# Optimization experiments

Measured on AMD Instinct MI355X. Metric: run time of the kernel, lower is better.

The kernel has to match this reference:

```python
import jax, jax.numpy as jnp
import numpy as np

QUERY_DIM = 1024
KEY_DIM = 768
NUM_HEADS = 16
HEAD_DIM = QUERY_DIM // NUM_HEADS
SCALE = HEAD_DIM ** -0.5


def setup_inputs() -> dict:
    key = jax.random.key(0)
    ks = jax.random.split(key, 11)
    B, Nq, Nk = 4, 4096, 1024
    s_q = QUERY_DIM ** -0.5
    s_k = KEY_DIM ** -0.5
    return {
        "query": jax.random.normal(ks[0], (B, Nq, QUERY_DIM), jnp.float32),
        "key": jax.random.normal(ks[1], (B, Nk, KEY_DIM), jnp.float32),
        "value": jax.random.normal(ks[2], (B, Nk, KEY_DIM), jnp.float32),
        "Wq": jax.random.normal(ks[3], (QUERY_DIM, QUERY_DIM), jnp.float32) * s_q,
        "bq": jnp.zeros((QUERY_DIM,), jnp.float32),
        "Wk": jax.random.normal(ks[4], (KEY_DIM, QUERY_DIM), jnp.float32) * s_k,
        "bk": jnp.zeros((QUERY_DIM,), jnp.float32),
        "Wv": jax.random.normal(ks[5], (KEY_DIM, QUERY_DIM), jnp.float32) * s_k,
        "bv": jnp.zeros((QUERY_DIM,), jnp.float32),
        "Wo": jax.random.normal(ks[6], (QUERY_DIM, QUERY_DIM), jnp.float32) * s_q,
        "bo": jnp.zeros((QUERY_DIM,), jnp.float32),
    }


def reference(query, key, value, Wq, bq, Wk, bk, Wv, bv, Wo, bo):
    B, Nq, _ = query.shape
    Nk = key.shape[1]
    # projections to (B, H, N, d)
    q = (query @ Wq + bq).reshape(B, Nq, NUM_HEADS, HEAD_DIM).transpose(0, 2, 1, 3)
    k = (key @ Wk + bk).reshape(B, Nk, NUM_HEADS, HEAD_DIM).transpose(0, 2, 1, 3)
    v = (value @ Wv + bv).reshape(B, Nk, NUM_HEADS, HEAD_DIM).transpose(0, 2, 1, 3)
    attn = jnp.einsum("bhqd,bhkd->bhqk", q, k) * SCALE
    attn = jax.nn.softmax(attn, axis=-1)
    out = jnp.einsum("bhqk,bhkd->bhqd", attn, v)
    out = out.transpose(0, 2, 1, 3).reshape(B, Nq, QUERY_DIM)
    return out @ Wo + bo
```

## Files before the change

### kernel.cpp

```cpp
#include <hip/hip_runtime.h>
#include <hip/hip_bf16.h>
#include <stdint.h>


typedef unsigned short u16;
typedef __attribute__((ext_vector_type(8))) short short8;
typedef __attribute__((ext_vector_type(4))) float f32x4;

#define B_SZ 4
#define NQ   4096
#define NK   1024
#define QDIM 1024
#define KDIM 768
#define NH   16
#define HD   64
#define QSCALE (0.125f * 1.44269504f)

__device__ __forceinline__ u16 f2bf(float f) {
  union { float f; uint32_t u; } v; v.f = f;
  uint32_t u = v.u;
  return (u16)((u + 0x7FFFu + ((u >> 16) & 1u)) >> 16);
}

__device__ __forceinline__ uint32_t pk2(float a, float b) {
  union { __hip_bfloat162 h; uint32_t u; } cv;
  cv.h = __float22bfloat162_rn(float2{a, b});
  return cv.u;
}

__device__ __forceinline__ float fexp2(float x) {
  return __builtin_amdgcn_exp2f(x);
}

__device__ __forceinline__ void async16(u16* lds, const u16* g) {
  __builtin_amdgcn_global_load_lds(
      (__attribute__((address_space(1))) void*)(g),
      (__attribute__((address_space(3))) void*)(lds), 16, 0, 0);
}

__global__ __launch_bounds__(256) void f32_to_bf16_k(const float* __restrict__ in,
                                                     u16* __restrict__ out, int n4) {
  int i = blockIdx.x * 256 + threadIdx.x;
  if (i < n4) {
    f32x4 v = ((const f32x4*)in)[i];
    uint2 o = {pk2(v.x, v.y), pk2(v.z, v.w)};
    ((uint2*)out)[i] = o;
  }
}

__global__ __launch_bounds__(256) void f32_to_bf16_2k(const float* __restrict__ a,
                                                      const float* __restrict__ b,
                                                      u16* __restrict__ oa,
                                                      u16* __restrict__ ob, int n4) {
  int i = blockIdx.x * 256 + threadIdx.x;
  const float* in = blockIdx.y ? b : a;
  u16* out = blockIdx.y ? ob : oa;
  if (i < n4) {
    f32x4 v = ((const f32x4*)in)[i];
    uint2 o = {pk2(v.x, v.y), pk2(v.z, v.w)};
    ((uint2*)out)[i] = o;
  }
}

__global__ __launch_bounds__(256) void transpose_bf16_k(const float* __restrict__ W,
                                                        u16* __restrict__ Wt,
                                                        int K, int N) {
  __shared__ float t[32][33];
  int tx = threadIdx.x & 31, ty = threadIdx.x >> 5;
  int nb = blockIdx.x * 32, kb = blockIdx.y * 32;
#pragma unroll
  for (int i = 0; i < 4; ++i)
    t[ty + i * 8][tx] = W[(size_t)(kb + ty + i * 8) * N + nb + tx];
  __syncthreads();
#pragma unroll
  for (int i = 0; i < 4; ++i)
    Wt[(size_t)(nb + ty + i * 8) * K + kb + tx] = f2bf(t[tx][ty + i * 8]);
}

__global__ __launch_bounds__(512, 2) void gemm_bt256(const u16* __restrict__ A,
                                                     const u16* __restrict__ Bt,
                                                     const float* __restrict__ bias,
                                                     float* __restrict__ Cf,
                                                     u16* __restrict__ Cb,
                                                     int M, int N, int K,
                                                     int out_bf16, float scale) {
  __shared__ __align__(16) u16 Al[3][128 * 64];
  __shared__ __align__(16) u16 Bl[3][256 * 64];
  const int tid = threadIdx.x;
  const int w = tid >> 6, lane = tid & 63;
  const int g = lane >> 4, l15 = lane & 15;
  const int sw = l15 & 7;
  const int mbase = blockIdx.x * 128, nbase = blockIdx.y * 256;
  const int wm = (w & 1) * 64, wn = (w >> 1) * 64;
  const int NT = K >> 6;

  const int ca0 = 0 * 512 + tid, ca1 = 1 * 512 + tid;
  const int ra0 = ca0 >> 3, rc0 = ((ca0 & 7) ^ (ra0 & 7)) * 8;
  const int ra1 = ca1 >> 3, rc1 = ((ca1 & 7) ^ (ra1 & 7)) * 8;
  const u16* pa0 = A + (size_t)(mbase + ra0) * K + rc0;
  const u16* pa1 = A + (size_t)(mbase + ra1) * K + rc1;
  const u16* pb[4];
#pragma unroll
  for (int i = 0; i < 4; ++i) {
    int c = i * 512 + tid;
    int row = c >> 3, col = ((c & 7) ^ (row & 7)) * 8;
    pb[i] = Bt + (size_t)(nbase + row) * K + col;
  }
  const int lA0 = (0 * 512 + w * 64) * 8, lA1 = (1 * 512 + w * 64) * 8;
  int lB[4];
#pragma unroll
  for (int i = 0; i < 4; ++i) lB[i] = (i * 512 + w * 64) * 8;

  f32x4 zero4 = {0.f, 0.f, 0.f, 0.f};
  f32x4 acc[4][4];
#pragma unroll
  for (int i = 0; i < 4; ++i)
#pragma unroll
    for (int j = 0; j < 4; ++j) acc[i][j] = zero4;

  async16(&Al[0][lA0], pa0); async16(&Al[0][lA1], pa1);
#pragma unroll
  for (int i = 0; i < 4; ++i) async16(&Bl[0][lB[i]], pb[i]);
  pa0 += 64; pa1 += 64;
#pragma unroll
  for (int i = 0; i < 4; ++i) pb[i] += 64;
  async16(&Al[1][lA0], pa0); async16(&Al[1][lA1], pa1);
#pragma unroll
  for (int i = 0; i < 4; ++i) async16(&Bl[1][lB[i]], pb[i]);
  pa0 += 64; pa1 += 64;
#pragma unroll
  for (int i = 0; i < 4; ++i) pb[i] += 64;
  asm volatile("s_waitcnt vmcnt(6)" ::: "memory");
  __builtin_amdgcn_sched_barrier(0);
  __builtin_amdgcn_s_barrier();

  int cb = 0, sb = 2;
  for (int kt = 0; kt < NT; ++kt) {
    const u16* Ap = &Al[cb][0];
    const u16* Bp = &Bl[cb][0];
    const bool st = (kt + 2 < NT);

    short8 af[4][2], bfa[2][2];
#pragma unroll
    for (int mt = 0; mt < 4; ++mt) {
      af[mt][0] = *(const short8*)&Ap[(wm + mt * 16 + l15) * 64 + (g ^ sw) * 8];
      af[mt][1] = *(const short8*)&Ap[(wm + mt * 16 + l15) * 64 + ((4 + g) ^ sw) * 8];
    }
#pragma unroll
    for (int nt = 0; nt < 2; ++nt) {
      bfa[nt][0] = *(const short8*)&Bp[(wn + nt * 16 + l15) * 64 + (g ^ sw) * 8];
      bfa[nt][1] = *(const short8*)&Bp[(wn + nt * 16 + l15) * 64 + ((4 + g) ^ sw) * 8];
    }
    if (st) {
      async16(&Al[sb][lA0], pa0);
      async16(&Al[sb][lA1], pa1);
      async16(&Bl[sb][lB[0]], pb[0]);
      async16(&Bl[sb][lB[1]], pb[1]);
    }
    __builtin_amdgcn_s_barrier();
    asm volatile("s_waitcnt lgkmcnt(0)" ::: "memory");
    __builtin_amdgcn_sched_barrier(0);
    __builtin_amdgcn_s_setprio(1);
#pragma unroll
    for (int ks = 0; ks < 2; ++ks)
#pragma unroll
      for (int mt = 0; mt < 4; ++mt)
#pragma unroll
        for (int nt = 0; nt < 2; ++nt)
          acc[mt][nt] = __builtin_amdgcn_mfma_f32_16x16x32_bf16(af[mt][ks], bfa[nt][ks],
                                                                acc[mt][nt], 0, 0, 0);
    __builtin_amdgcn_s_setprio(0);
    __builtin_amdgcn_s_barrier();

    short8 bfb[2][2];
#pragma unroll
    for (int nt = 0; nt < 2; ++nt) {
      bfb[nt][0] = *(const short8*)&Bp[(wn + (nt + 2) * 16 + l15) * 64 + (g ^ sw) * 8];
      bfb[nt][1] = *(const short8*)&Bp[(wn + (nt + 2) * 16 + l15) * 64 + ((4 + g) ^ sw) * 8];
    }
    if (st) {
      async16(&Bl[sb][lB[2]], pb[2]);
      async16(&Bl[sb][lB[3]], pb[3]);
      pa0 += 64; pa1 += 64;
#pragma unroll
      for (int i = 0; i < 4; ++i) pb[i] += 64;
    }
    __builtin_amdgcn_s_barrier();
    asm volatile("s_waitcnt lgkmcnt(0)" ::: "memory");
    __builtin_amdgcn_sched_barrier(0);
    __builtin_amdgcn_s_setprio(1);
#pragma unroll
    for (int ks = 0; ks < 2; ++ks)
#pragma unroll
      for (int mt = 0; mt < 4; ++mt)
#pragma unroll
        for (int nt = 0; nt < 2; ++nt)
          acc[mt][nt + 2] = __builtin_amdgcn_mfma_f32_16x16x32_bf16(af[mt][ks], bfb[nt][ks],
                                                                    acc[mt][nt + 2], 0, 0, 0);
    __builtin_amdgcn_s_setprio(0);

    if (kt < NT - 2) {
      asm volatile("s_waitcnt vmcnt(6)" ::: "memory");
    } else if (kt == NT - 2) {
      asm volatile("s_waitcnt vmcnt(0)" ::: "memory");
    }
    __builtin_amdgcn_sched_barrier(0);
    __builtin_amdgcn_s_barrier();
    cb = (cb == 2) ? 0 : cb + 1;
    sb = (sb == 2) ? 0 : sb + 1;
  }

#pragma unroll
  for (int nt = 0; nt < 4; ++nt) {
    int col = nbase + wn + nt * 16 + l15;
    float bv = bias[col];
#pragma unroll
    for (int mt = 0; mt < 4; ++mt)
#pragma unroll
      for (int r = 0; r < 4; ++r) {
        int row = mbase + wm + mt * 16 + g * 4 + r;
        float v = (acc[mt][nt][r] + bv) * scale;
        if (out_bf16) Cb[(size_t)row * N + col] = f2bf(v);
        else          Cf[(size_t)row * N + col] = v;
      }
  }
}

__global__ __launch_bounds__(256) void gemm_kv(const u16* __restrict__ kA,
                                               const u16* __restrict__ vA,
                                               const u16* __restrict__ Wk,
                                               const u16* __restrict__ Wv,
                                               const float* __restrict__ bk,
                                               const float* __restrict__ bv,
                                               u16* __restrict__ Kp,
                                               u16* __restrict__ VT,
                                               int M, int N, int K) {
  __shared__ __align__(16) u16 Al[128 * 64];
  __shared__ __align__(16) u16 Bl[128 * 64];
  const int ct = blockIdx.z;
  const u16* A  = ct ? vA : kA;
  const u16* Bt = ct ? Wv : Wk;
  const float* bias = ct ? bv : bk;
  const int tid = threadIdx.x;
  const int w = tid >> 6, lane = tid & 63;
  const int g = lane >> 4, l15 = lane & 15;
  const int sw = l15 & 7;
  const int mbase = blockIdx.x * 128, nbase = blockIdx.y * 128;
  const int wm = (w & 1) * 64, wn = (w >> 1) * 64;

  f32x4 zero4 = {0.f, 0.f, 0.f, 0.f};
  f32x4 acc[4][4];
#pragma unroll
  for (int i = 0; i < 4; ++i)
#pragma unroll
    for (int j = 0; j < 4; ++j) acc[i][j] = zero4;

  for (int kb = 0; kb < K; kb += 64) {
#pragma unroll
    for (int i = 0; i < 4; ++i) {
      int cbase = w * 256 + i * 64;
      int c = cbase + lane;
      int row = c >> 3;
      int kc8 = ((c & 7) ^ (row & 7)) * 8;
      async16(&Al[cbase * 8], A + (size_t)(mbase + row) * K + kb + kc8);
      async16(&Bl[cbase * 8], Bt + (size_t)(nbase + row) * K + kb + kc8);
    }
    __syncthreads();
#pragma unroll
    for (int ks = 0; ks < 2; ++ks) {
      short8 af[4], bf[4];
#pragma unroll
      for (int mt = 0; mt < 4; ++mt)
        af[mt] = *(const short8*)&Al[(wm + mt * 16 + l15) * 64 + ((ks * 4 + g) ^ sw) * 8];
#pragma unroll
      for (int nt = 0; nt < 4; ++nt)
        bf[nt] = *(const short8*)&Bl[(wn + nt * 16 + l15) * 64 + ((ks * 4 + g) ^ sw) * 8];
      if (ct) {
#pragma unroll
        for (int nt = 0; nt < 4; ++nt)
#pragma unroll
          for (int mt = 0; mt < 4; ++mt)
            acc[nt][mt] = __builtin_amdgcn_mfma_f32_16x16x32_bf16(bf[nt], af[mt],
                                                                  acc[nt][mt], 0, 0, 0);
      } else {
#pragma unroll
        for (int mt = 0; mt < 4; ++mt)
#pragma unroll
          for (int nt = 0; nt < 4; ++nt)
            acc[mt][nt] = __builtin_amdgcn_mfma_f32_16x16x32_bf16(af[mt], bf[nt],
                                                                  acc[mt][nt], 0, 0, 0);
      }
    }
    __syncthreads();
  }

  if (ct) {
#pragma unroll
    for (int mt = 0; mt < 4; ++mt) {
      int m = mbase + wm + mt * 16 + l15;
#pragma unroll
      for (int nt = 0; nt < 4; ++nt)
#pragma unroll
        for (int r = 0; r < 4; ++r) {
          int n = nbase + wn + nt * 16 + g * 4 + r;
          VT[(size_t)n * M + m] = f2bf(acc[nt][mt][r] + bias[n]);
        }
    }
  } else {
#pragma unroll
    for (int nt = 0; nt < 4; ++nt) {
      int col = nbase + wn + nt * 16 + l15;
      float bvv = bias[col];
#pragma unroll
      for (int mt = 0; mt < 4; ++mt)
#pragma unroll
        for (int r = 0; r < 4; ++r) {
          int row = mbase + wm + mt * 16 + g * 4 + r;
          Kp[(size_t)row * N + col] = f2bf(acc[mt][nt][r] + bvv);
        }
    }
  }
}

__global__ __launch_bounds__(256, 2) void attn_kernel(const u16* __restrict__ Qp,
                                                      const u16* __restrict__ Kp,
                                                      const u16* __restrict__ VT,
                                                      u16* __restrict__ AO) {
  __shared__ __align__(16) u16 K_lds[2][64 * 64];
  __shared__ __align__(16) u16 V_lds[3][64 * 64];
  __shared__ __align__(16) u16 P_lds[4][32 * 64];

  const int tid = threadIdx.x;
  const int w = tid >> 6, lane = tid & 63;
  const int g = lane >> 4, l15 = lane & 15;
  const int sw = l15 & 7;
  const int bh = blockIdx.y, b = bh >> 4, h = bh & 15;
  const int qrow0 = blockIdx.x * 128 + w * 32;
  const int MT = B_SZ * NK;

  const int cbase0 = (w * 2 + 0) * 64;
  const int cbase1 = (w * 2 + 1) * 64;
  const int c0 = cbase0 + lane, c1 = cbase1 + lane;
  const int row0 = c0 >> 3, kc80 = ((c0 & 7) ^ (row0 & 7)) * 8;
  const int row1 = c1 >> 3, kc81 = ((c1 & 7) ^ (row1 & 7)) * 8;

  const u16* kp0 = Kp + (size_t)(b * NK + row0) * QDIM + h * HD + kc80;
  const u16* kp1 = Kp + (size_t)(b * NK + row1) * QDIM + h * HD + kc81;
  const u16* vp0 = VT + (size_t)(h * HD + row0) * MT + b * NK + kc80;
  const u16* vp1 = VT + (size_t)(h * HD + row1) * MT + b * NK + kc81;

  const int rb = l15 * 64;
  const int cs0 = (g ^ sw) * 8;
  const int cs1 = ((4 + g) ^ sw) * 8;
  const int pwb = rb + (((g >> 1) ^ (sw & 1)) * 8) + (g & 1) * 4;
  const int pms = sw & 6;

  short8 ones8;
#pragma unroll
  for (int j = 0; j < 8; ++j) ones8[j] = (short)0x3F80;

  short8 qf[2][2];
#pragma unroll
  for (int qt = 0; qt < 2; ++qt)
#pragma unroll
    for (int ks = 0; ks < 2; ++ks) {
      size_t row = (size_t)(b * NQ + qrow0 + qt * 16 + l15);
      qf[qt][ks] = *(const short8*)(Qp + row * QDIM + h * HD + ks * 32 + g * 8);
    }

  f32x4 zero4 = {0.f, 0.f, 0.f, 0.f};
  f32x4 o4[4][2];
  f32x4 lacc[2];
#pragma unroll
  for (int dt = 0; dt < 4; ++dt)
#pragma unroll
    for (int qt = 0; qt < 2; ++qt) o4[dt][qt] = zero4;
  lacc[0] = zero4; lacc[1] = zero4;

  u16* Pl = &P_lds[w][0];

  async16(&K_lds[0][cbase0 * 8], kp0);
  async16(&K_lds[0][cbase1 * 8], kp1);
  async16(&V_lds[0][cbase0 * 8], vp0);
  async16(&V_lds[0][cbase1 * 8], vp1);
  kp0 += 64 * QDIM; kp1 += 64 * QDIM; vp0 += 64; vp1 += 64;
  __syncthreads();

  async16(&K_lds[1][cbase0 * 8], kp0);
  async16(&K_lds[1][cbase1 * 8], kp1);
  async16(&V_lds[1][cbase0 * 8], vp0);
  async16(&V_lds[1][cbase1 * 8], vp1);
  kp0 += 64 * QDIM; kp1 += 64 * QDIM; vp0 += 64; vp1 += 64;

  {
    const u16* Kl = &K_lds[0][0];
    f32x4 sc[4][2];
    short8 kf0[4], kf1[4];
#pragma unroll
    for (int mt = 0; mt < 4; ++mt) {
      kf0[mt] = *(const short8*)&Kl[mt * 1024 + rb + cs0];
      kf1[mt] = *(const short8*)&Kl[mt * 1024 + rb + cs1];
    }
    __builtin_amdgcn_s_setprio(1);
#pragma unroll
    for (int mt = 0; mt < 4; ++mt)
#pragma unroll
      for (int qt = 0; qt < 2; ++qt)
        sc[mt][qt] = __builtin_amdgcn_mfma_f32_16x16x32_bf16(kf0[mt], qf[qt][0],
                                                             zero4, 0, 0, 0);
#pragma unroll
    for (int mt = 0; mt < 4; ++mt)
#pragma unroll
      for (int qt = 0; qt < 2; ++qt)
        sc[mt][qt] = __builtin_amdgcn_mfma_f32_16x16x32_bf16(kf1[mt], qf[qt][1],
                                                             sc[mt][qt], 0, 0, 0);
    __builtin_amdgcn_s_setprio(0);
#pragma unroll
    for (int qt = 0; qt < 2; ++qt)
#pragma unroll
      for (int mt = 0; mt < 4; ++mt) {
        float p0 = fexp2(sc[mt][qt][0]);
        float p1 = fexp2(sc[mt][qt][1]);
        float p2 = fexp2(sc[mt][qt][2]);
        float p3 = fexp2(sc[mt][qt][3]);
        uint2 pk = {pk2(p0, p1), pk2(p2, p3)};
        *(uint2*)&Pl[qt * 1024 + pwb + ((mt * 2) ^ pms) * 8] = pk;
      }
  }
  __syncthreads();

  for (int kc = 1; kc < NK / 64; ++kc) {
    const int pv = (kc - 1) % 3;
    if (kc + 1 < NK / 64) {
      const int nk = (kc + 1) & 1, nv = (kc + 1) % 3;
      async16(&K_lds[nk][cbase0 * 8], kp0);
      async16(&K_lds[nk][cbase1 * 8], kp1);
      async16(&V_lds[nv][cbase0 * 8], vp0);
      async16(&V_lds[nv][cbase1 * 8], vp1);
      kp0 += 64 * QDIM; kp1 += 64 * QDIM; vp0 += 64; vp1 += 64;
    }
    const u16* Kl = &K_lds[kc & 1][0];
    const u16* Vl = &V_lds[pv][0];

    short8 pb[2][2], vf[2][4], kf[2][4];
#pragma unroll
    for (int qt = 0; qt < 2; ++qt) {
      pb[0][qt] = *(const short8*)&Pl[qt * 1024 + rb + cs0];
      pb[1][qt] = *(const short8*)&Pl[qt * 1024 + rb + cs1];
    }
#pragma unroll
    for (int dt = 0; dt < 4; ++dt) {
      vf[0][dt] = *(const short8*)&Vl[dt * 1024 + rb + cs0];
      vf[1][dt] = *(const short8*)&Vl[dt * 1024 + rb + cs1];
    }
#pragma unroll
    for (int mt = 0; mt < 4; ++mt) {
      kf[0][mt] = *(const short8*)&Kl[mt * 1024 + rb + cs0];
      kf[1][mt] = *(const short8*)&Kl[mt * 1024 + rb + cs1];
    }

    f32x4 sc[4][2];
    __builtin_amdgcn_s_setprio(1);
#pragma unroll
    for (int mt = 0; mt < 4; ++mt)
#pragma unroll
      for (int qt = 0; qt < 2; ++qt)
        sc[mt][qt] = __builtin_amdgcn_mfma_f32_16x16x32_bf16(kf[0][mt], qf[qt][0],
                                                             zero4, 0, 0, 0);
#pragma unroll
    for (int qt = 0; qt < 2; ++qt)
      lacc[qt] = __builtin_amdgcn_mfma_f32_16x16x32_bf16(ones8, pb[0][qt],
                                                         lacc[qt], 0, 0, 0);
#pragma unroll
    for (int dt = 0; dt < 4; ++dt)
#pragma unroll
      for (int qt = 0; qt < 2; ++qt)
        o4[dt][qt] = __builtin_amdgcn_mfma_f32_16x16x32_bf16(vf[0][dt], pb[0][qt],
                                                             o4[dt][qt], 0, 0, 0);
#pragma unroll
    for (int mt = 0; mt < 4; ++mt)
#pragma unroll
      for (int qt = 0; qt < 2; ++qt)
        sc[mt][qt] = __builtin_amdgcn_mfma_f32_16x16x32_bf16(kf[1][mt], qf[qt][1],
                                                             sc[mt][qt], 0, 0, 0);
#pragma unroll
    for (int qt = 0; qt < 2; ++qt)
      lacc[qt] = __builtin_amdgcn_mfma_f32_16x16x32_bf16(ones8, pb[1][qt],
                                                         lacc[qt], 0, 0, 0);
#pragma unroll
    for (int dt = 0; dt < 4; ++dt)
#pragma unroll
      for (int qt = 0; qt < 2; ++qt)
        o4[dt][qt] = __builtin_amdgcn_mfma_f32_16x16x32_bf16(vf[1][dt], pb[1][qt],
                                                             o4[dt][qt], 0, 0, 0);
    __builtin_amdgcn_s_setprio(0);

#pragma unroll
    for (int qt = 0; qt < 2; ++qt)
#pragma unroll
      for (int mt = 0; mt < 4; ++mt) {
        float p0 = fexp2(sc[mt][qt][0]);
        float p1 = fexp2(sc[mt][qt][1]);
        float p2 = fexp2(sc[mt][qt][2]);
        float p3 = fexp2(sc[mt][qt][3]);
        uint2 pk = {pk2(p0, p1), pk2(p2, p3)};
        *(uint2*)&Pl[qt * 1024 + pwb + ((mt * 2) ^ pms) * 8] = pk;
      }

    asm volatile("s_waitcnt vmcnt(2)" ::: "memory");
    __builtin_amdgcn_sched_barrier(0);
    __builtin_amdgcn_s_barrier();
  }

  asm volatile("s_waitcnt vmcnt(0)" ::: "memory");
  __builtin_amdgcn_sched_barrier(0);
  __builtin_amdgcn_s_barrier();

  {
    const u16* Vl = &V_lds[(NK / 64 - 1) % 3][0];
    short8 pb[2][2], vf[2][4];
#pragma unroll
    for (int qt = 0; qt < 2; ++qt) {
      pb[0][qt] = *(const short8*)&Pl[qt * 1024 + rb + cs0];
      pb[1][qt] = *(const short8*)&Pl[qt * 1024 + rb + cs1];
    }
#pragma unroll
    for (int dt = 0; dt < 4; ++dt) {
      vf[0][dt] = *(const short8*)&Vl[dt * 1024 + rb + cs0];
      vf[1][dt] = *(const short8*)&Vl[dt * 1024 + rb + cs1];
    }
    __builtin_amdgcn_s_setprio(1);
#pragma unroll
    for (int ks = 0; ks < 2; ++ks) {
#pragma unroll
      for (int qt = 0; qt < 2; ++qt)
        lacc[qt] = __builtin_amdgcn_mfma_f32_16x16x32_bf16(ones8, pb[ks][qt],
                                                           lacc[qt], 0, 0, 0);
#pragma unroll
      for (int dt = 0; dt < 4; ++dt)
#pragma unroll
        for (int qt = 0; qt < 2; ++qt)
          o4[dt][qt] = __builtin_amdgcn_mfma_f32_16x16x32_bf16(vf[ks][dt], pb[ks][qt],
                                                               o4[dt][qt], 0, 0, 0);
    }
    __builtin_amdgcn_s_setprio(0);
  }

#pragma unroll
  for (int qt = 0; qt < 2; ++qt) {
    float inv = __builtin_amdgcn_rcpf(lacc[qt][0]);
    size_t row = (size_t)(b * NQ + qrow0 + qt * 16 + l15);
#pragma unroll
    for (int dt = 0; dt < 4; ++dt) {
      uint2 pk = {pk2(o4[dt][qt][0] * inv, o4[dt][qt][1] * inv),
                  pk2(o4[dt][qt][2] * inv, o4[dt][qt][3] * inv)};
      *(uint2*)(AO + row * QDIM + h * HD + dt * 16 + g * 4) = pk;
    }
  }
}

extern "C" void kernel_launch(void* const* d_in, const int* in_sizes, int n_in,
                              void* d_out, int out_size, void* d_ws, size_t ws_size,
                              hipStream_t stream) {
  const float* query = (const float*)d_in[0];
  const float* key   = (const float*)d_in[1];
  const float* value = (const float*)d_in[2];
  const float* Wq = (const float*)d_in[3];
  const float* bq = (const float*)d_in[4];
  const float* Wk = (const float*)d_in[5];
  const float* bk = (const float*)d_in[6];
  const float* Wv = (const float*)d_in[7];
  const float* bv = (const float*)d_in[8];
  const float* Wo = (const float*)d_in[9];
  const float* bo = (const float*)d_in[10];

  char* ws = (char*)d_ws;
  size_t off = 0;
  auto alloc = [&](size_t bytes) -> void* {
    void* p = ws + off;
    off += (bytes + 255) & ~(size_t)255;
    return p;
  };
  const size_t NQTOT = (size_t)B_SZ * NQ;
  const size_t NKTOT = (size_t)B_SZ * NK;
  u16* qbf = (u16*)alloc(NQTOT * QDIM * 2);
  u16* kbf = (u16*)alloc(NKTOT * KDIM * 2);
  u16* vbf = (u16*)alloc(NKTOT * KDIM * 2);
  u16* wqt = (u16*)alloc((size_t)QDIM * QDIM * 2);
  u16* wkt = (u16*)alloc((size_t)KDIM * QDIM * 2);
  u16* wvt = (u16*)alloc((size_t)KDIM * QDIM * 2);
  u16* wot = (u16*)alloc((size_t)QDIM * QDIM * 2);
  u16* Qp  = (u16*)alloc(NQTOT * QDIM * 2);
  u16* Kp  = (u16*)alloc(NKTOT * QDIM * 2);
  u16* VT  = (u16*)alloc((size_t)QDIM * NKTOT * 2);
  u16* AO  = qbf;

  {
    int n4 = (int)(NQTOT * QDIM / 4);
    f32_to_bf16_k<<<(n4 + 255) / 256, 256, 0, stream>>>(query, qbf, n4);
  }
  {
    int n4 = (int)(NKTOT * KDIM / 4);
    f32_to_bf16_2k<<<dim3((n4 + 255) / 256, 2), 256, 0, stream>>>(key, value, kbf,
                                                                  vbf, n4);
  }
  transpose_bf16_k<<<dim3(QDIM / 32, QDIM / 32), 256, 0, stream>>>(Wq, wqt, QDIM, QDIM);
  transpose_bf16_k<<<dim3(QDIM / 32, KDIM / 32), 256, 0, stream>>>(Wk, wkt, KDIM, QDIM);
  transpose_bf16_k<<<dim3(QDIM / 32, KDIM / 32), 256, 0, stream>>>(Wv, wvt, KDIM, QDIM);
  transpose_bf16_k<<<dim3(QDIM / 32, QDIM / 32), 256, 0, stream>>>(Wo, wot, QDIM, QDIM);

  gemm_bt256<<<dim3(NQTOT / 128, QDIM / 256), 512, 0, stream>>>(
      qbf, wqt, bq, nullptr, Qp, (int)NQTOT, QDIM, QDIM, 1, QSCALE);
  gemm_kv<<<dim3(NKTOT / 128, QDIM / 128, 2), 256, 0, stream>>>(
      kbf, vbf, wkt, wvt, bk, bv, Kp, VT, (int)NKTOT, QDIM, KDIM);

  attn_kernel<<<dim3(NQ / 128, B_SZ * NH), 256, 0, stream>>>(Qp, Kp, VT, AO);

  gemm_bt256<<<dim3(NQTOT / 128, QDIM / 256), 512, 0, stream>>>(
      AO, wot, bo, (float*)d_out, nullptr, (int)NQTOT, QDIM, QDIM, 0, 1.0f);

  (void)in_sizes; (void)n_in; (void)out_size; (void)ws_size;
}
```

Baseline: 415.4 us.

## Merge conversion/transpose launches and swizzle GEMM block order across XCDs

Combines the query/key/value bf16 conversions into one launch and the four weight transposes into one 3D launch, reducing the number of kernel launches. Also flattens the GEMM grids to 1D and remaps block IDs so that consecutive blocks on the same XCD (bid&7 grouping) cover neighbouring tiles, which should improve L2 reuse of A/B tiles. Transpose blocks with kb beyond KDIM for Wk/Wv exit early, at the cost of some wasted block launches.

```diff
diff --git a/kernel.cpp b/kernel.cpp
--- a/kernel.cpp
+++ b/kernel.cpp
@@ -38,43 +38,48 @@
       (__attribute__((address_space(3))) void*)(lds), 16, 0, 0);
 }
 
-__global__ __launch_bounds__(256) void f32_to_bf16_k(const float* __restrict__ in,
-                                                     u16* __restrict__ out, int n4) {
+__global__ __launch_bounds__(256) void f32_to_bf16_all(const float* __restrict__ q,
+                                                       const float* __restrict__ k,
+                                                       const float* __restrict__ v,
+                                                       u16* __restrict__ oq,
+                                                       u16* __restrict__ ok,
+                                                       u16* __restrict__ ov,
+                                                       int n4q, int n4kv) {
   int i = blockIdx.x * 256 + threadIdx.x;
-  if (i < n4) {
-    f32x4 v = ((const f32x4*)in)[i];
-    uint2 o = {pk2(v.x, v.y), pk2(v.z, v.w)};
-    ((uint2*)out)[i] = o;
-  }
-}
-
-__global__ __launch_bounds__(256) void f32_to_bf16_2k(const float* __restrict__ a,
-                                                      const float* __restrict__ b,
-                                                      u16* __restrict__ oa,
-                                                      u16* __restrict__ ob, int n4) {
-  int i = blockIdx.x * 256 + threadIdx.x;
-  const float* in = blockIdx.y ? b : a;
-  u16* out = blockIdx.y ? ob : oa;
-  if (i < n4) {
-    f32x4 v = ((const f32x4*)in)[i];
-    uint2 o = {pk2(v.x, v.y), pk2(v.z, v.w)};
-    ((uint2*)out)[i] = o;
-  }
-}
-
-__global__ __launch_bounds__(256) void transpose_bf16_k(const float* __restrict__ W,
-                                                        u16* __restrict__ Wt,
-                                                        int K, int N) {
+  const float* in; u16* out; int idx;
+  if (i < n4q) { in = q; out = oq; idx = i; }
+  else if (i < n4q + n4kv) { in = k; out = ok; idx = i - n4q; }
+  else if (i < n4q + 2 * n4kv) { in = v; out = ov; idx = i - n4q - n4kv; }
+  else return;
+  f32x4 vv = ((const f32x4*)in)[idx];
+  uint2 o = {pk2(vv.x, vv.y), pk2(vv.z, vv.w)};
+  ((uint2*)out)[idx] = o;
+}
+
+__global__ __launch_bounds__(256) void transpose4_k(const float* __restrict__ W0,
+                                                    const float* __restrict__ W1,
+                                                    const float* __restrict__ W2,
+                                                    const float* __restrict__ W3,
+                                                    u16* __restrict__ T0,
+                                                    u16* __restrict__ T1,
+                                                    u16* __restrict__ T2,
+                                                    u16* __restrict__ T3) {
+  const int z = blockIdx.z;
+  const float* W = (z == 0) ? W0 : (z == 1) ? W1 : (z == 2) ? W2 : W3;
+  u16* T = (z == 0) ? T0 : (z == 1) ? T1 : (z == 2) ? T2 : T3;
+  const int K = (z == 1 || z == 2) ? KDIM : QDIM;
+  const int N = QDIM;
+  int nb = blockIdx.x * 32, kb = blockIdx.y * 32;
+  if (kb >= K) return;
   __shared__ float t[32][33];
   int tx = threadIdx.x & 31, ty = threadIdx.x >> 5;
-  int nb = blockIdx.x * 32, kb = blockIdx.y * 32;
 #pragma unroll
   for (int i = 0; i < 4; ++i)
     t[ty + i * 8][tx] = W[(size_t)(kb + ty + i * 8) * N + nb + tx];
   __syncthreads();
 #pragma unroll
   for (int i = 0; i < 4; ++i)
-    Wt[(size_t)(nb + ty + i * 8) * K + kb + tx] = f2bf(t[tx][ty + i * 8]);
+    T[(size_t)(nb + ty + i * 8) * K + kb + tx] = f2bf(t[tx][ty + i * 8]);
 }
 
 __global__ __launch_bounds__(512, 2) void gemm_bt256(const u16* __restrict__ A,
@@ -90,7 +95,11 @@
   const int w = tid >> 6, lane = tid & 63;
   const int g = lane >> 4, l15 = lane & 15;
   const int sw = l15 & 7;
-  const int mbase = blockIdx.x * 128, nbase = blockIdx.y * 256;
+  const int bid = blockIdx.x;
+  const int cpx = gridDim.x >> 3;
+  const int swz = (bid & 7) * cpx + (bid >> 3);
+  const int nby = N >> 8;
+  const int mbase = (swz / nby) * 128, nbase = (swz % nby) * 256;
   const int wm = (w & 1) * 64, wn = (w >> 1) * 64;
   const int NT = K >> 6;
 
@@ -237,7 +246,10 @@
                                                int M, int N, int K) {
   __shared__ __align__(16) u16 Al[128 * 64];
   __shared__ __align__(16) u16 Bl[128 * 64];
-  const int ct = blockIdx.z;
+  const int bid = blockIdx.x;
+  const int swz = (bid & 7) * 64 + (bid >> 3);
+  const int ct = swz >> 8;
+  const int mbase = (swz & 31) * 128, nbase = ((swz >> 5) & 7) * 128;
   const u16* A  = ct ? vA : kA;
   const u16* Bt = ct ? Wv : Wk;
   const float* bias = ct ? bv : bk;
@@ -245,7 +257,6 @@
   const int w = tid >> 6, lane = tid & 63;
   const int g = lane >> 4, l15 = lane & 15;
   const int sw = l15 & 7;
-  const int mbase = blockIdx.x * 128, nbase = blockIdx.y * 128;
   const int wm = (w & 1) * 64, wn = (w >> 1) * 64;
 
   f32x4 zero4 = {0.f, 0.f, 0.f, 0.f};
@@ -596,27 +607,23 @@
   u16* AO  = qbf;
 
   {
-    int n4 = (int)(NQTOT * QDIM / 4);
-    f32_to_bf16_k<<<(n4 + 255) / 256, 256, 0, stream>>>(query, qbf, n4);
-  }
-  {
-    int n4 = (int)(NKTOT * KDIM / 4);
-    f32_to_bf16_2k<<<dim3((n4 + 255) / 256, 2), 256, 0, stream>>>(key, value, kbf,
-                                                                  vbf, n4);
-  }
-  transpose_bf16_k<<<dim3(QDIM / 32, QDIM / 32), 256, 0, stream>>>(Wq, wqt, QDIM, QDIM);
-  transpose_bf16_k<<<dim3(QDIM / 32, KDIM / 32), 256, 0, stream>>>(Wk, wkt, KDIM, QDIM);
-  transpose_bf16_k<<<dim3(QDIM / 32, KDIM / 32), 256, 0, stream>>>(Wv, wvt, KDIM, QDIM);
-  transpose_bf16_k<<<dim3(QDIM / 32, QDIM / 32), 256, 0, stream>>>(Wo, wot, QDIM, QDIM);
-
-  gemm_bt256<<<dim3(NQTOT / 128, QDIM / 256), 512, 0, stream>>>(
+    int n4q  = (int)(NQTOT * QDIM / 4);
+    int n4kv = (int)(NKTOT * KDIM / 4);
+    int nb = (n4q + 2 * n4kv + 255) / 256;
+    f32_to_bf16_all<<<nb, 256, 0, stream>>>(query, key, value, qbf, kbf, vbf,
+                                            n4q, n4kv);
+  }
+  transpose4_k<<<dim3(QDIM / 32, QDIM / 32, 4), 256, 0, stream>>>(
+      Wq, Wk, Wv, Wo, wqt, wkt, wvt, wot);
+
+  gemm_bt256<<<(NQTOT / 128) * (QDIM / 256), 512, 0, stream>>>(
       qbf, wqt, bq, nullptr, Qp, (int)NQTOT, QDIM, QDIM, 1, QSCALE);
-  gemm_kv<<<dim3(NKTOT / 128, QDIM / 128, 2), 256, 0, stream>>>(
+  gemm_kv<<<(NKTOT / 128) * (QDIM / 128) * 2, 256, 0, stream>>>(
       kbf, vbf, wkt, wvt, bk, bv, Kp, VT, (int)NKTOT, QDIM, KDIM);
 
   attn_kernel<<<dim3(NQ / 128, B_SZ * NH), 256, 0, stream>>>(Qp, Kp, VT, AO);
 
-  gemm_bt256<<<dim3(NQTOT / 128, QDIM / 256), 512, 0, stream>>>(
+  gemm_bt256<<<(NQTOT / 128) * (QDIM / 256), 512, 0, stream>>>(
       AO, wot, bo, (float*)d_out, nullptr, (int)NQTOT, QDIM, QDIM, 0, 1.0f);
 
   (void)in_sizes; (void)n_in; (void)out_size; (void)ws_size;
```

New measurement: 392.1 us. 1.06x faster.
